# Performance work log

Measured on AMD Instinct MI355X. Metric: run time of the kernel, lower is better.

## Reference

```python
import jax, jax.numpy as jnp
import numpy as np
import math

B, S, D, H = 4, 1024, 2048, 16
DH = D // H          # dim_head = 128
DHID = 128           # dim_hid
DKER = 64            # dim_ker
EPS = 1e-6


def setup_inputs() -> dict:
    key = jax.random.key(0)
    ks = jax.random.split(key, 12)
    a1 = math.sqrt(6.0 / (DH + DHID))
    a2 = math.sqrt(6.0 / (DKER + DHID))
    a3 = math.sqrt(6.0 / (2 * DKER))
    return {
        "q": jax.random.normal(ks[0], (B, S, D), jnp.float32),
        "k": jax.random.normal(ks[1], (B, S, D), jnp.float32),
        "v": jax.random.normal(ks[2], (B, S, D), jnp.float32),
        "lr_attn_mask": jax.random.randint(ks[3], (B, 1, S, S), 0, 2).astype(bool),
        "sparse_norms_lse": jax.random.normal(ks[4], (B, H, S, 1), jnp.float32),
        "sparse_attn_weights": jax.random.normal(ks[5], (B, H, S, S), jnp.float32),
        "kernel_q_mat1": jax.random.uniform(ks[6], (H, DH, DHID), jnp.float32, -a1, a1),
        "kernel_k_mat1": jax.random.uniform(ks[7], (H, DH, DHID), jnp.float32, -a1, a1),
        "kernel_q_mat2": jax.random.uniform(ks[8], (H, DHID, DKER), jnp.float32, -a2, a2),
        "kernel_k_mat2": jax.random.uniform(ks[9], (H, DHID, DKER), jnp.float32, -a2, a2),
        "interaction_k": jax.random.uniform(ks[10], (H, DKER, DKER), jnp.float32, -a3, a3),
        "scalingD": jnp.ones((1, H, 1, DKER), jnp.float32) * 1e-4,
        "scalingD2": jnp.ones((1, H, 1, DKER), jnp.float32) * 1e-4,
        "lambda_constant": 1,
    }


def _gelu(x):
    # torch F.gelu default = exact (erf) gelu
    return jax.nn.gelu(x, approximate=False)


def reference(q, k, v, lr_attn_mask, sparse_norms_lse, sparse_attn_weights,
              kernel_q_mat1, kernel_k_mat1, kernel_q_mat2, kernel_k_mat2,
              interaction_k, scalingD, scalingD2, lambda_constant):
    # split heads: [B,S,D] -> [B,H,S,DH]
    qh = q.reshape(B, S, H, DH).transpose(0, 2, 1, 3)
    kh = k.reshape(B, S, H, DH).transpose(0, 2, 1, 3)
    vh = v.reshape(B, S, H, DH).transpose(0, 2, 1, 3)

    # learned kernel feature maps (dropout=0 -> identity)
    qf = _gelu(jnp.einsum('bhsd,hde->bhse', qh, kernel_q_mat1))
    qf = _gelu(jnp.einsum('bhse,hef->bhsf', qf, kernel_q_mat2))

    kf = _gelu(jnp.einsum('bhsd,hde->bhse', kh, kernel_k_mat1))
    kf = jnp.abs(scalingD) * _gelu(jnp.einsum('bhse,hef->bhsf', kf, kernel_k_mat2))
    kf = kf + jnp.einsum('bhse,hef->bhsf', kf, interaction_k) * scalingD2

    # low-rank (kernelized) scores, masked. [B,H,S,S]
    scores = jnp.einsum('bhse,bhte->bhst', jnp.abs(qf), jnp.abs(kf))
    m = lr_attn_mask.astype(scores.dtype)  # [B,1,S,S] broadcasts
    scores = m * scores

    # log-domain merge with external sparse attention
    lr_norms_lse = jnp.log(scores.sum(axis=-1, keepdims=True) + EPS)
    norm_factor_lse = jnp.logaddexp(lr_norms_lse, sparse_norms_lse)
    logits = jnp.log(scores + EPS) * m + (1.0 - m) * sparse_attn_weights
    attn = jnp.exp(logits - norm_factor_lse)

    out = jnp.einsum('bhst,bhtd->bhsd', attn, vh)
    return out.transpose(0, 2, 1, 3).reshape(B, S, D)
```

## Files before the change

kernel.cpp:

```cpp
#include <hip/hip_runtime.h>


typedef __bf16 bf16_t;
typedef __attribute__((ext_vector_type(8))) __bf16 bf16x8;
typedef __attribute__((ext_vector_type(4))) float f32x4;

#define MFMA(a, b, c) __builtin_amdgcn_mfma_f32_16x16x32_bf16((a), (b), (c), 0, 0, 0)

typedef __attribute__((address_space(3))) void as3_void;
typedef __attribute__((address_space(1))) const void as1_void;
static __device__ __forceinline__ void gload16(const void* g, void* l) {
    __builtin_amdgcn_global_load_lds((as1_void*)g, (as3_void*)l, 16, 0, 0);
}

static __device__ __forceinline__ float gelu_exact(float x) {
    return 0.5f * x * (1.0f + erff(x * 0.70710678118654752f));
}

static __device__ __forceinline__ unsigned pack_bf16(float a, float b) {
    bf16_t x = (bf16_t)a, y = (bf16_t)b;
    unsigned short ux = __builtin_bit_cast(unsigned short, x);
    unsigned short uy = __builtin_bit_cast(unsigned short, y);
    return (unsigned)ux | ((unsigned)uy << 16);
}

__global__ __launch_bounds__(256) void conv_weights_kernel(
    const float* __restrict__ wq1, const float* __restrict__ wk1,
    const float* __restrict__ wq2, const float* __restrict__ wk2,
    const float* __restrict__ iK,
    bf16_t* __restrict__ wq1t, bf16_t* __restrict__ wk1t,
    bf16_t* __restrict__ wq2t, bf16_t* __restrict__ wk2t,
    bf16_t* __restrict__ iKt)
{
    const int idx = blockIdx.x * 256 + threadIdx.x;
    if (idx < 16 * 128 * 128) {
        int h = idx >> 14, e = (idx >> 7) & 127, d = idx & 127;
        wq1t[idx] = (bf16_t)wq1[(h << 14) + (d << 7) + e];
        wk1t[idx] = (bf16_t)wk1[(h << 14) + (d << 7) + e];
    }
    if (idx < 16 * 64 * 128) {
        int h = idx >> 13, f = (idx >> 7) & 63, e = idx & 127;
        wq2t[idx] = (bf16_t)wq2[(h << 13) + (e << 6) + f];
        wk2t[idx] = (bf16_t)wk2[(h << 13) + (e << 6) + f];
    }
    if (idx < 16 * 64 * 64) {
        int h = idx >> 12, g = (idx >> 6) & 63, f = idx & 63;
        iKt[idx] = (bf16_t)iK[(h << 12) + (f << 6) + g];
    }
}

__global__ __launch_bounds__(256) void prep_kernel(
    const float* __restrict__ q, const float* __restrict__ k,
    const float* __restrict__ v, const unsigned char* __restrict__ mask8,
    const bf16_t* __restrict__ wq1t, const bf16_t* __restrict__ wq2t,
    const bf16_t* __restrict__ wk1t, const bf16_t* __restrict__ wk2t,
    const bf16_t* __restrict__ iKt,
    const float* __restrict__ sD, const float* __restrict__ sD2,
    bf16_t* __restrict__ qf, bf16_t* __restrict__ kf,
    bf16_t* __restrict__ vT, unsigned char* __restrict__ mprep)
{
    __shared__ char smem[44032];
    const int bxg = blockIdx.x;
    const int tid = threadIdx.x;

    if (bxg < 1024) {
        __shared__ int mflag;
        if (tid == 0) {
            unsigned a = 0;
            for (int i = 0; i < 64; ++i) a |= mask8[4 * i + 1];
            mflag = (a == 0) ? 1 : 0;
        }
        __syncthreads();
        const size_t base = ((size_t)bxg * 256 + tid) * 16;
        if (mflag) {
            const int* mi = (const int*)mask8;
            uint4 r;
            unsigned bs[4];
#pragma unroll
            for (int j = 0; j < 4; ++j) {
                int4 vv = *reinterpret_cast<const int4*>(&mi[base + j * 4]);
                bs[j] = (vv.x ? 1u : 0u) | ((vv.y ? 1u : 0u) << 8) |
                        ((vv.z ? 1u : 0u) << 16) | ((vv.w ? 1u : 0u) << 24);
            }
            r.x = bs[0]; r.y = bs[1]; r.z = bs[2]; r.w = bs[3];
            *reinterpret_cast<uint4*>(&mprep[base]) = r;
        } else {
            uint4 vv = *reinterpret_cast<const uint4*>(&mask8[base]);
            uint4 r;
            unsigned* pv = (unsigned*)&vv;
            unsigned* pr = (unsigned*)&r;
#pragma unroll
            for (int j = 0; j < 4; ++j) {
                unsigned x = pv[j], o = 0;
#pragma unroll
                for (int kk = 0; kk < 4; ++kk)
                    o |= (((x >> (8 * kk)) & 255u) ? 1u : 0u) << (8 * kk);
                pr[j] = o;
            }
            *reinterpret_cast<uint4*>(&mprep[base]) = r;
        }
        return;
    }

    if (bxg < 2048) {
        typedef bf16_t tr_t[72];
        tr_t* tr = reinterpret_cast<tr_t*>(smem);
        const int idv = bxg - 1024;
        const int bh = idv & 63, b = bh >> 4, h = bh & 15;
        const int tt = idv >> 6;
        const int t0 = tt * 64;
#pragma unroll
        for (int i = 0; i < 8; ++i) {
            int f4 = tid + 256 * i;
            int t = f4 >> 5, c4 = f4 & 31;
            const float4 vv = *reinterpret_cast<const float4*>(
                &v[((size_t)b * 1024 + t0 + t) * 2048 + h * 128 + c4 * 4]);
            tr[c4 * 4 + 0][t] = (bf16_t)vv.x;
            tr[c4 * 4 + 1][t] = (bf16_t)vv.y;
            tr[c4 * 4 + 2][t] = (bf16_t)vv.z;
            tr[c4 * 4 + 3][t] = (bf16_t)vv.w;
        }
        __syncthreads();
#pragma unroll
        for (int i = 0; i < 32; ++i) {
            int e = tid + 256 * i;
            int d = e >> 6, tl = e & 63;
            vT[(((size_t)bh * 16 + tt) * 128 + d) * 64 + tl] = tr[d][tl];
        }
        return;
    }

    {
        typedef bf16_t row136[136];
        typedef bf16_t row72[72];
        row136* xa = reinterpret_cast<row136*>(smem);
        row136* h1 = reinterpret_cast<row136*>(smem + 17408);
        row72*  k2 = reinterpret_cast<row72*>(smem + 34816);

        const int idf = bxg - 2048;
        const int lane = tid & 63, w = tid >> 6;
        const int lr = lane & 15, lg = lane >> 4;
        const int row0 = (idf & 63) * 64;
        const int h = (idf >> 6) & 15;
        const int path = idf >> 10;

        const float* X = path ? k : q;
        const bf16_t* w1t = path ? wk1t : wq1t;
        const bf16_t* w2t = path ? wk2t : wq2t;
        bf16_t* outp = path ? kf : qf;

#pragma unroll
        for (int i = 0; i < 8; ++i) {
            int f4 = tid + 256 * i;
            int r = f4 >> 5, c4 = f4 & 31;
            const float4 vv = *reinterpret_cast<const float4*>(
                &X[(size_t)(row0 + r) * 2048 + h * 128 + c4 * 4]);
            xa[r][c4 * 4 + 0] = (bf16_t)vv.x;
            xa[r][c4 * 4 + 1] = (bf16_t)vv.y;
            xa[r][c4 * 4 + 2] = (bf16_t)vv.z;
            xa[r][c4 * 4 + 3] = (bf16_t)vv.w;
        }
        __syncthreads();

        bf16x8 a1[4];
#pragma unroll
        for (int kk = 0; kk < 4; ++kk)
            a1[kk] = *reinterpret_cast<const bf16x8*>(&xa[w * 16 + lr][kk * 32 + lg * 8]);
#pragma unroll
        for (int nt = 0; nt < 8; ++nt) {
            f32x4 acc = {0.f, 0.f, 0.f, 0.f};
#pragma unroll
            for (int kk = 0; kk < 4; ++kk) {
                bf16x8 bfr = *reinterpret_cast<const bf16x8*>(
                    &w1t[(size_t)h * 16384 + (nt * 16 + lr) * 128 + kk * 32 + lg * 8]);
                acc = MFMA(a1[kk], bfr, acc);
            }
#pragma unroll
            for (int r = 0; r < 4; ++r)
                h1[w * 16 + lg * 4 + r][nt * 16 + lr] = (bf16_t)gelu_exact(acc[r]);
        }
        __syncthreads();

        bf16x8 a2[4];
#pragma unroll
        for (int kk = 0; kk < 4; ++kk)
            a2[kk] = *reinterpret_cast<const bf16x8*>(&h1[w * 16 + lr][kk * 32 + lg * 8]);

        if (path == 0) {
#pragma unroll
            for (int nt = 0; nt < 4; ++nt) {
                f32x4 acc = {0.f, 0.f, 0.f, 0.f};
#pragma unroll
                for (int kk = 0; kk < 4; ++kk) {
                    bf16x8 bfr = *reinterpret_cast<const bf16x8*>(
                        &w2t[(size_t)h * 8192 + (nt * 16 + lr) * 128 + kk * 32 + lg * 8]);
                    acc = MFMA(a2[kk], bfr, acc);
                }
#pragma unroll
                for (int r = 0; r < 4; ++r) {
                    int n = row0 + w * 16 + lg * 4 + r;
                    int bb = n >> 10, s = n & 1023;
                    outp[(((size_t)bb * 16 + h) * 1024 + s) * 64 + nt * 16 + lr] =
                        (bf16_t)fabsf(gelu_exact(acc[r]));
                }
            }
        } else {
#pragma unroll
            for (int nt = 0; nt < 4; ++nt) {
                f32x4 acc = {0.f, 0.f, 0.f, 0.f};
#pragma unroll
                for (int kk = 0; kk < 4; ++kk) {
                    bf16x8 bfr = *reinterpret_cast<const bf16x8*>(
                        &w2t[(size_t)h * 8192 + (nt * 16 + lr) * 128 + kk * 32 + lg * 8]);
                    acc = MFMA(a2[kk], bfr, acc);
                }
#pragma unroll
                for (int r = 0; r < 4; ++r) {
                    int f = nt * 16 + lr;
                    k2[w * 16 + lg * 4 + r][f] =
                        (bf16_t)(fabsf(sD[h * 64 + f]) * gelu_exact(acc[r]));
                }
            }
            __syncthreads();
            bf16x8 a3[2];
#pragma unroll
            for (int kk = 0; kk < 2; ++kk)
                a3[kk] = *reinterpret_cast<const bf16x8*>(&k2[w * 16 + lr][kk * 32 + lg * 8]);
#pragma unroll
            for (int nt = 0; nt < 4; ++nt) {
                f32x4 acc = {0.f, 0.f, 0.f, 0.f};
#pragma unroll
                for (int kk = 0; kk < 2; ++kk) {
                    bf16x8 bfr = *reinterpret_cast<const bf16x8*>(
                        &iKt[(size_t)h * 4096 + (nt * 16 + lr) * 64 + kk * 32 + lg * 8]);
                    acc = MFMA(a3[kk], bfr, acc);
                }
#pragma unroll
                for (int r = 0; r < 4; ++r) {
                    int row = w * 16 + lg * 4 + r;
                    int g = nt * 16 + lr;
                    float base = (float)k2[row][g];
                    float kv = fabsf(base + acc[r] * sD2[h * 64 + g]);
                    int n = row0 + row;
                    int bb = n >> 10, s = n & 1023;
                    outp[(((size_t)bb * 16 + h) * 1024 + s) * 64 + g] = (bf16_t)kv;
                }
            }
        }
    }
}

__global__ __launch_bounds__(256, 3) void attn_cv_kernel(
    const bf16_t* __restrict__ qf, const bf16_t* __restrict__ kf,
    const bf16_t* __restrict__ vT,
    const unsigned char* __restrict__ mprep,
    const float* __restrict__ saw, const float* __restrict__ lse,
    float* __restrict__ out)
{
    __shared__ bf16_t vbuf[3][128 * 64];

    const int tid = threadIdx.x;
    const int lane = tid & 63, w = tid >> 6;
    const int lr = lane & 15, lg = lane >> 4;

    const int di = blockIdx.y * 16 + blockIdx.x;
    const int xcd = di & 7, rr = di >> 3;
    const int bh = xcd + 8 * (rr >> 4);
    const int s0 = (rr & 15) * 64;
    const int b = bh >> 4, h = bh & 15;

    const int srow = s0 + w * 16 + lr;
    const size_t saw_row = ((size_t)bh << 20) + (size_t)srow * 1024;
    const size_t m_row   = ((size_t)b << 20) + (size_t)srow * 1024;

    const int vrow = tid >> 3;
    const int vcol8 = (tid & 7) ^ (vrow & 7);
    const bf16_t* vt_bh = vT + (size_t)bh * 131072;
    const bf16_t* kf_bh = kf + (size_t)bh * 65536;

    bf16x8 aq0, aq1;
    {
        const size_t qb = ((size_t)bh * 1024 + srow) * 64;
        aq0 = *reinterpret_cast<const bf16x8*>(&qf[qb + lg * 8]);
        aq1 = *reinterpret_cast<const bf16x8*>(&qf[qb + 32 + lg * 8]);
    }

    const f32x4 fzero = {0.f, 0.f, 0.f, 0.f};
    f32x4 oacc[8];
#pragma unroll
    for (int i = 0; i < 8; ++i) oacc[i] = fzero;
    float rs = 0.f;


#define STAGE_VT(BUF, TILE)                                                      \
    {                                                                            \
        const bf16_t* vg = vt_bh + (size_t)(TILE) * 8192 + vcol8 * 8;            \
        char* lb = (char*)&vbuf[BUF][0] + w * 1024;                              \
        _Pragma("unroll")                                                        \
        for (int j = 0; j < 4; ++j)                                              \
            gload16(vg + (size_t)(32 * j + vrow) * 64, lb + j * 4096);           \
    }

#define LOAD_KF(TILE, KR)                                                        \
    {                                                                            \
        _Pragma("unroll")                                                        \
        for (int nt = 0; nt < 4; ++nt) {                                         \
            const size_t kb = ((size_t)(TILE) * 64 + nt * 16 + lr) * 64;         \
            KR[nt * 2]     = *reinterpret_cast<const bf16x8*>(&kf_bh[kb + lg * 8]); \
            KR[nt * 2 + 1] = *reinterpret_cast<const bf16x8*>(&kf_bh[kb + 32 + lg * 8]); \
        }                                                                        \
    }

#define LOAD_SAW(TILE, SS, MM)                                                   \
    {                                                                            \
        _Pragma("unroll")                                                        \
        for (int nt = 0; nt < 4; ++nt) {                                         \
            SS[nt] = *reinterpret_cast<const f32x4*>(                            \
                &saw[saw_row + (size_t)(TILE) * 64 + nt * 16 + lg * 4]);         \
            MM[nt] = *reinterpret_cast<const unsigned*>(                         \
                &mprep[m_row + (size_t)(TILE) * 64 + nt * 16 + lg * 4]);         \
        }                                                                        \
    }

#define QKT_MERGE(KR, SS, MM)                                                    \
    {                                                                            \
        _Pragma("unroll")                                                        \
        for (int nt = 0; nt < 4; ++nt) {                                         \
            f32x4 acc = fzero;                                                   \
            acc = MFMA(KR[nt * 2], aq0, acc);                                    \
            acc = MFMA(KR[nt * 2 + 1], aq1, acc);                                \
            const unsigned mm = MM[nt];                                          \
            float v0, v1, v2, v3;                                                \
            v0 = (mm & 255u)         ? (acc[0] + 1e-6f) : __expf(SS[nt][0]);     \
            rs += (mm & 255u)         ? acc[0] : 0.f;                            \
            v1 = ((mm >> 8) & 255u)  ? (acc[1] + 1e-6f) : __expf(SS[nt][1]);     \
            rs += ((mm >> 8) & 255u)  ? acc[1] : 0.f;                            \
            v2 = ((mm >> 16) & 255u) ? (acc[2] + 1e-6f) : __expf(SS[nt][2]);     \
            rs += ((mm >> 16) & 255u) ? acc[2] : 0.f;                            \
            v3 = (mm >> 24)          ? (acc[3] + 1e-6f) : __expf(SS[nt][3]);     \
            rs += (mm >> 24)          ? acc[3] : 0.f;                            \
            pk[nt * 2]     = pack_bf16(v0, v1);                                  \
            pk[nt * 2 + 1] = pack_bf16(v2, v3);                                  \
        }                                                                        \
    }

#define REDIST()                                                                 \
    {                                                                            \
        const int srcA = lr + ((lg & 1) << 5);                                   \
        const int srcB = srcA + 16;                                              \
        const bool sel = (lg < 2);                                               \
        const unsigned a0 = __shfl(pk[0], srcA, 64);                             \
        const unsigned a1 = __shfl(pk[1], srcA, 64);                             \
        const unsigned a2 = __shfl(pk[2], srcA, 64);                             \
        const unsigned a3 = __shfl(pk[3], srcA, 64);                             \
        const unsigned b0 = __shfl(pk[0], srcB, 64);                             \
        const unsigned b1 = __shfl(pk[1], srcB, 64);                             \
        const unsigned b2 = __shfl(pk[2], srcB, 64);                             \
        const unsigned b3 = __shfl(pk[3], srcB, 64);                             \
        f0w.x = sel ? a0 : a2;  f0w.y = sel ? a1 : a3;                           \
        f0w.z = sel ? b0 : b2;  f0w.w = sel ? b1 : b3;                           \
        const unsigned c4 = __shfl(pk[4], srcA, 64);                             \
        const unsigned c5 = __shfl(pk[5], srcA, 64);                             \
        const unsigned c6 = __shfl(pk[6], srcA, 64);                             \
        const unsigned c7 = __shfl(pk[7], srcA, 64);                             \
        const unsigned d4 = __shfl(pk[4], srcB, 64);                             \
        const unsigned d5 = __shfl(pk[5], srcB, 64);                             \
        const unsigned d6 = __shfl(pk[6], srcB, 64);                             \
        const unsigned d7 = __shfl(pk[7], srcB, 64);                             \
        f1w.x = sel ? c4 : c6;  f1w.y = sel ? c5 : c7;                           \
        f1w.z = sel ? d4 : d6;  f1w.w = sel ? d5 : d7;                           \
    }

#define PV(CUR)                                                                  \
    {                                                                            \
        bf16x8 pf0 = __builtin_bit_cast(bf16x8, f0w);                            \
        bf16x8 pf1 = __builtin_bit_cast(bf16x8, f1w);                            \
        __builtin_amdgcn_s_setprio(1);                                           \
        _Pragma("unroll")                                                        \
        for (int dt = 0; dt < 8; ++dt) {                                         \
            const int row = dt * 16 + lr;                                        \
            const char* vb = (const char*)&vbuf[CUR][0] + row * 128;             \
            const int sw = (row & 7) * 16;                                       \
            bf16x8 v0 = *reinterpret_cast<const bf16x8*>(vb + ((lg * 16) ^ sw)); \
            bf16x8 v1 = *reinterpret_cast<const bf16x8*>(vb + ((64 + lg * 16) ^ sw)); \
            oacc[dt] = MFMA(v0, pf0, oacc[dt]);                                  \
            oacc[dt] = MFMA(v1, pf1, oacc[dt]);                                  \
        }                                                                        \
        __builtin_amdgcn_s_setprio(0);                                           \
    }

#define FULL_PHASE(CIDX, SIDX, I, KRC, SSC, MMC, KRN, SSN, MMN)                  \
    {                                                                            \
        LOAD_KF((I) + 1, KRN);                                                   \
        LOAD_SAW((I) + 1, SSN, MMN);                                             \
        STAGE_VT(SIDX, (I) + 2);                                                 \
        __builtin_amdgcn_sched_barrier(0);                                       \
        asm volatile("s_waitcnt vmcnt(24)" ::: "memory");                        \
        __builtin_amdgcn_s_barrier();                                            \
        __builtin_amdgcn_sched_barrier(0);                                       \
        QKT_MERGE(KRC, SSC, MMC);                                                \
        REDIST();                                                                \
        __builtin_amdgcn_sched_barrier(0);                                       \
        PV(CIDX);                                                                \
        __builtin_amdgcn_sched_barrier(0);                                       \
        __builtin_amdgcn_s_barrier();                                            \
    }

    f32x4 sawA[4], sawB[4];
    unsigned muA[4], muB[4];
    bf16x8 kfA[8], kfB[8];
    unsigned pk[8];
    uint4 f0w, f1w;

    LOAD_KF(0, kfA);
    LOAD_SAW(0, sawA, muA);
    STAGE_VT(0, 0);
    STAGE_VT(1, 1);

    int c0 = 0, c1 = 1, c2 = 2;
    for (int i = 0; i < 14; i += 2) {
        FULL_PHASE(c0, c2, i,     kfA, sawA, muA, kfB, sawB, muB);
        FULL_PHASE(c1, c0, i + 1, kfB, sawB, muB, kfA, sawA, muA);
        const int t_ = c0; c0 = c2; c2 = c1; c1 = t_;
    }

    {
        LOAD_KF(15, kfB);
        LOAD_SAW(15, sawB, muB);
        __builtin_amdgcn_sched_barrier(0);
        asm volatile("s_waitcnt vmcnt(20)" ::: "memory");
        __builtin_amdgcn_s_barrier();
        __builtin_amdgcn_sched_barrier(0);
        QKT_MERGE(kfA, sawA, muA);
        REDIST();
        __builtin_amdgcn_sched_barrier(0);
        PV(c0);
        __builtin_amdgcn_sched_barrier(0);
        __builtin_amdgcn_s_barrier();
    }
    {
        asm volatile("s_waitcnt vmcnt(0)" ::: "memory");
        __builtin_amdgcn_s_barrier();
        __builtin_amdgcn_sched_barrier(0);
        QKT_MERGE(kfB, sawB, muB);
        REDIST();
        __builtin_amdgcn_sched_barrier(0);
        PV(c1);
    }

    rs += __shfl_xor(rs, 16);
    rs += __shfl_xor(rs, 32);
    const float invden =
        1.0f / (rs + 1e-6f + __expf(lse[(size_t)bh * 1024 + srow]));

    const size_t ob = ((size_t)b * 1024 + srow) * 2048 + h * 128 + lg * 4;
#pragma unroll
    for (int dt = 0; dt < 8; ++dt) {
        f32x4 o;
        o[0] = oacc[dt][0] * invden;
        o[1] = oacc[dt][1] * invden;
        o[2] = oacc[dt][2] * invden;
        o[3] = oacc[dt][3] * invden;
        *reinterpret_cast<f32x4*>(&out[ob + dt * 16]) = o;
    }
#undef STAGE_VT
#undef LOAD_KF
#undef LOAD_SAW
#undef QKT_MERGE
#undef REDIST
#undef PV
#undef FULL_PHASE
}

extern "C" void kernel_launch(void* const* d_in, const int* in_sizes, int n_in,
                              void* d_out, int out_size, void* d_ws, size_t ws_size,
                              hipStream_t stream)
{
    const float* q   = (const float*)d_in[0];
    const float* k   = (const float*)d_in[1];
    const float* v   = (const float*)d_in[2];
    const unsigned char* mask = (const unsigned char*)d_in[3];
    const float* lse = (const float*)d_in[4];
    const float* saw = (const float*)d_in[5];
    const float* wq1 = (const float*)d_in[6];
    const float* wk1 = (const float*)d_in[7];
    const float* wq2 = (const float*)d_in[8];
    const float* wk2 = (const float*)d_in[9];
    const float* iK  = (const float*)d_in[10];
    const float* sD  = (const float*)d_in[11];
    const float* sD2 = (const float*)d_in[12];
    float* out = (float*)d_out;

    bf16_t* wsb  = (bf16_t*)d_ws;
    bf16_t* wq1t = wsb;
    bf16_t* wk1t = wq1t + 262144;
    bf16_t* wq2t = wk1t + 262144;
    bf16_t* wk2t = wq2t + 131072;
    bf16_t* iKt  = wk2t + 131072;
    bf16_t* qf   = iKt  + 65536;
    bf16_t* kf   = qf   + 4194304;
    bf16_t* vT   = kf   + 4194304;
    unsigned char* mprep = (unsigned char*)(vT + 8388608);

    conv_weights_kernel<<<dim3(1024), dim3(256), 0, stream>>>(
        wq1, wk1, wq2, wk2, iK, wq1t, wk1t, wq2t, wk2t, iKt);
    prep_kernel<<<dim3(4096), dim3(256), 0, stream>>>(
        q, k, v, mask, wq1t, wq2t, wk1t, wk2t, iKt, sD, sD2, qf, kf, vT, mprep);
    attn_cv_kernel<<<dim3(16, 64), dim3(256), 0, stream>>>(
        qf, kf, vT, mprep, saw, lse, out);
}
```

Before: 232.6 us.

## Precompute exp of sparse weights merged with mask into bf16 tile layout

The prep kernel now reads the fp32 sparse attention weights and the mask once. It writes a single bf16 tensor in a tiled layout: exp(weight) where the mask is off, and a -1 sentinel where the mask is on. The attention kernel then loads this compact bf16 tensor instead of the fp32 weights plus a separate mask byte array, and drops its per-element exp. This halves the bytes the attention loop has to stream, but the extra write and read-back of the intermediate raises total global memory traffic. Storing exp values in bf16 also adds rounding error.

```diff
diff --git a/kernel.cpp b/kernel.cpp
--- a/kernel.cpp
+++ b/kernel.cpp
@@ -22,6 +22,10 @@
     unsigned short ux = __builtin_bit_cast(unsigned short, x);
     unsigned short uy = __builtin_bit_cast(unsigned short, y);
     return (unsigned)ux | ((unsigned)uy << 16);
+}
+
+static __device__ __forceinline__ float bf16u_to_f32(unsigned short u) {
+    return __uint_as_float((unsigned)u << 16);
 }
 
 __global__ __launch_bounds__(256) void conv_weights_kernel(
@@ -52,12 +56,13 @@
 __global__ __launch_bounds__(256) void prep_kernel(
     const float* __restrict__ q, const float* __restrict__ k,
     const float* __restrict__ v, const unsigned char* __restrict__ mask8,
+    const float* __restrict__ saw,
     const bf16_t* __restrict__ wq1t, const bf16_t* __restrict__ wq2t,
     const bf16_t* __restrict__ wk1t, const bf16_t* __restrict__ wk2t,
     const bf16_t* __restrict__ iKt,
     const float* __restrict__ sD, const float* __restrict__ sD2,
     bf16_t* __restrict__ qf, bf16_t* __restrict__ kf,
-    bf16_t* __restrict__ vT, unsigned char* __restrict__ mprep)
+    bf16_t* __restrict__ vT, bf16_t* __restrict__ pt)
 {
     __shared__ char smem[44032];
     const int bxg = blockIdx.x;
@@ -71,33 +76,41 @@
             mflag = (a == 0) ? 1 : 0;
         }
         __syncthreads();
-        const size_t base = ((size_t)bxg * 256 + tid) * 16;
-        if (mflag) {
-            const int* mi = (const int*)mask8;
-            uint4 r;
-            unsigned bs[4];
-#pragma unroll
-            for (int j = 0; j < 4; ++j) {
-                int4 vv = *reinterpret_cast<const int4*>(&mi[base + j * 4]);
-                bs[j] = (vv.x ? 1u : 0u) | ((vv.y ? 1u : 0u) << 8) |
-                        ((vv.z ? 1u : 0u) << 16) | ((vv.w ? 1u : 0u) << 24);
+        const bool mask_is_int = (mflag != 0);
+        const int* mask32 = (const int*)mask8;
+
+        const int bh = bxg & 63, b = bh >> 4;
+        const int s0 = (bxg >> 6) * 64;
+        const int w_ = tid >> 6, l = tid & 63;
+        const size_t sawb = ((size_t)bh << 20) + (size_t)s0 * 1024;
+        const size_t mb = ((size_t)b << 20) + (size_t)s0 * 1024;
+
+        for (int tc = 0; tc < 4; ++tc) {
+#pragma unroll
+            for (int i = 0; i < 16; ++i) {
+                const int r = i * 4 + w_;
+                const int col = tc * 256 + l * 4;
+                const size_t e = (size_t)r * 1024 + col;
+                const float4 sv = *reinterpret_cast<const float4*>(&saw[sawb + e]);
+                int m0, m1, m2, m3;
+                if (mask_is_int) {
+                    const int4 mv = *reinterpret_cast<const int4*>(&mask32[mb + e]);
+                    m0 = mv.x; m1 = mv.y; m2 = mv.z; m3 = mv.w;
+                } else {
+                    const uchar4 mv = *reinterpret_cast<const uchar4*>(&mask8[mb + e]);
+                    m0 = mv.x; m1 = mv.y; m2 = mv.z; m3 = mv.w;
+                }
+                bf16_t o[4];
+                o[0] = m0 ? (bf16_t)(-1.0f) : (bf16_t)__expf(sv.x);
+                o[1] = m1 ? (bf16_t)(-1.0f) : (bf16_t)__expf(sv.y);
+                o[2] = m2 ? (bf16_t)(-1.0f) : (bf16_t)__expf(sv.z);
+                o[3] = m3 ? (bf16_t)(-1.0f) : (bf16_t)__expf(sv.w);
+                const int ttg = tc * 4 + (l >> 4);
+                const int tin = (l & 15) * 4;
+                *reinterpret_cast<uint2*>(
+                    &pt[(((size_t)bh * 16 + ttg) * 1024 + s0 + r) * 64 + tin]) =
+                    *reinterpret_cast<const uint2*>(o);
             }
-            r.x = bs[0]; r.y = bs[1]; r.z = bs[2]; r.w = bs[3];
-            *reinterpret_cast<uint4*>(&mprep[base]) = r;
-        } else {
-            uint4 vv = *reinterpret_cast<const uint4*>(&mask8[base]);
-            uint4 r;
-            unsigned* pv = (unsigned*)&vv;
-            unsigned* pr = (unsigned*)&r;
-#pragma unroll
-            for (int j = 0; j < 4; ++j) {
-                unsigned x = pv[j], o = 0;
-#pragma unroll
-                for (int kk = 0; kk < 4; ++kk)
-                    o |= (((x >> (8 * kk)) & 255u) ? 1u : 0u) << (8 * kk);
-                pr[j] = o;
-            }
-            *reinterpret_cast<uint4*>(&mprep[base]) = r;
         }
         return;
     }
@@ -252,10 +265,8 @@
 
 __global__ __launch_bounds__(256, 3) void attn_cv_kernel(
     const bf16_t* __restrict__ qf, const bf16_t* __restrict__ kf,
-    const bf16_t* __restrict__ vT,
-    const unsigned char* __restrict__ mprep,
-    const float* __restrict__ saw, const float* __restrict__ lse,
-    float* __restrict__ out)
+    const bf16_t* __restrict__ vT, const bf16_t* __restrict__ pt,
+    const float* __restrict__ lse, float* __restrict__ out)
 {
     __shared__ bf16_t vbuf[3][128 * 64];
 
@@ -270,13 +281,13 @@
     const int b = bh >> 4, h = bh & 15;
 
     const int srow = s0 + w * 16 + lr;
-    const size_t saw_row = ((size_t)bh << 20) + (size_t)srow * 1024;
-    const size_t m_row   = ((size_t)b << 20) + (size_t)srow * 1024;
 
     const int vrow = tid >> 3;
     const int vcol8 = (tid & 7) ^ (vrow & 7);
     const bf16_t* vt_bh = vT + (size_t)bh * 131072;
     const bf16_t* kf_bh = kf + (size_t)bh * 65536;
+    const unsigned short* ptp = (const unsigned short*)pt
+        + ((size_t)bh * 16) * 65536 + (size_t)srow * 64;
 
     bf16x8 aq0, aq1;
     {
@@ -311,34 +322,34 @@
         }                                                                        \
     }
 
-#define LOAD_SAW(TILE, SS, MM)                                                   \
+#define LOAD_PT(TILE, PP)                                                        \
     {                                                                            \
         _Pragma("unroll")                                                        \
-        for (int nt = 0; nt < 4; ++nt) {                                         \
-            SS[nt] = *reinterpret_cast<const f32x4*>(                            \
-                &saw[saw_row + (size_t)(TILE) * 64 + nt * 16 + lg * 4]);         \
-            MM[nt] = *reinterpret_cast<const unsigned*>(                         \
-                &mprep[m_row + (size_t)(TILE) * 64 + nt * 16 + lg * 4]);         \
-        }                                                                        \
-    }
-
-#define QKT_MERGE(KR, SS, MM)                                                    \
+        for (int nt = 0; nt < 4; ++nt)                                           \
+            PP[nt] = *reinterpret_cast<const ushort4*>(                          \
+                &ptp[(size_t)(TILE) * 65536 + nt * 16 + lg * 4]);                \
+    }
+
+#define QKT_MERGE(KR, PP)                                                        \
     {                                                                            \
         _Pragma("unroll")                                                        \
         for (int nt = 0; nt < 4; ++nt) {                                         \
             f32x4 acc = fzero;                                                   \
             acc = MFMA(KR[nt * 2], aq0, acc);                                    \
             acc = MFMA(KR[nt * 2 + 1], aq1, acc);                                \
-            const unsigned mm = MM[nt];                                          \
+            const float pe0 = bf16u_to_f32(PP[nt].x);                            \
+            const float pe1 = bf16u_to_f32(PP[nt].y);                            \
+            const float pe2 = bf16u_to_f32(PP[nt].z);                            \
+            const float pe3 = bf16u_to_f32(PP[nt].w);                            \
             float v0, v1, v2, v3;                                                \
-            v0 = (mm & 255u)         ? (acc[0] + 1e-6f) : __expf(SS[nt][0]);     \
-            rs += (mm & 255u)         ? acc[0] : 0.f;                            \
-            v1 = ((mm >> 8) & 255u)  ? (acc[1] + 1e-6f) : __expf(SS[nt][1]);     \
-            rs += ((mm >> 8) & 255u)  ? acc[1] : 0.f;                            \
-            v2 = ((mm >> 16) & 255u) ? (acc[2] + 1e-6f) : __expf(SS[nt][2]);     \
-            rs += ((mm >> 16) & 255u) ? acc[2] : 0.f;                            \
-            v3 = (mm >> 24)          ? (acc[3] + 1e-6f) : __expf(SS[nt][3]);     \
-            rs += (mm >> 24)          ? acc[3] : 0.f;                            \
+            v0 = (pe0 < 0.f) ? (acc[0] + 1e-6f) : pe0;                           \
+            rs += (pe0 < 0.f) ? acc[0] : 0.f;                                    \
+            v1 = (pe1 < 0.f) ? (acc[1] + 1e-6f) : pe1;                           \
+            rs += (pe1 < 0.f) ? acc[1] : 0.f;                                    \
+            v2 = (pe2 < 0.f) ? (acc[2] + 1e-6f) : pe2;                           \
+            rs += (pe2 < 0.f) ? acc[2] : 0.f;                                    \
+            v3 = (pe3 < 0.f) ? (acc[3] + 1e-6f) : pe3;                           \
+            rs += (pe3 < 0.f) ? acc[3] : 0.f;                                    \
             pk[nt * 2]     = pack_bf16(v0, v1);                                  \
             pk[nt * 2 + 1] = pack_bf16(v2, v3);                                  \
         }                                                                        \
@@ -389,16 +400,16 @@
         __builtin_amdgcn_s_setprio(0);                                           \
     }
 
-#define FULL_PHASE(CIDX, SIDX, I, KRC, SSC, MMC, KRN, SSN, MMN)                  \
+#define FULL_PHASE(CIDX, SIDX, I, KRC, PPC, KRN, PPN)                            \
     {                                                                            \
         LOAD_KF((I) + 1, KRN);                                                   \
-        LOAD_SAW((I) + 1, SSN, MMN);                                             \
+        LOAD_PT((I) + 1, PPN);                                                   \
         STAGE_VT(SIDX, (I) + 2);                                                 \
         __builtin_amdgcn_sched_barrier(0);                                       \
-        asm volatile("s_waitcnt vmcnt(24)" ::: "memory");                        \
+        asm volatile("s_waitcnt vmcnt(20)" ::: "memory");                        \
         __builtin_amdgcn_s_barrier();                                            \
         __builtin_amdgcn_sched_barrier(0);                                       \
-        QKT_MERGE(KRC, SSC, MMC);                                                \
+        QKT_MERGE(KRC, PPC);                                                     \
         REDIST();                                                                \
         __builtin_amdgcn_sched_barrier(0);                                       \
         PV(CIDX);                                                                \
@@ -406,32 +417,31 @@
         __builtin_amdgcn_s_barrier();                                            \
     }
 
-    f32x4 sawA[4], sawB[4];
-    unsigned muA[4], muB[4];
+    ushort4 ptA[4], ptB[4];
     bf16x8 kfA[8], kfB[8];
     unsigned pk[8];
     uint4 f0w, f1w;
 
     LOAD_KF(0, kfA);
-    LOAD_SAW(0, sawA, muA);
+    LOAD_PT(0, ptA);
     STAGE_VT(0, 0);
     STAGE_VT(1, 1);
 
     int c0 = 0, c1 = 1, c2 = 2;
     for (int i = 0; i < 14; i += 2) {
-        FULL_PHASE(c0, c2, i,     kfA, sawA, muA, kfB, sawB, muB);
-        FULL_PHASE(c1, c0, i + 1, kfB, sawB, muB, kfA, sawA, muA);
+        FULL_PHASE(c0, c2, i,     kfA, ptA, kfB, ptB);
+        FULL_PHASE(c1, c0, i + 1, kfB, ptB, kfA, ptA);
         const int t_ = c0; c0 = c2; c2 = c1; c1 = t_;
     }
 
     {
         LOAD_KF(15, kfB);
-        LOAD_SAW(15, sawB, muB);
+        LOAD_PT(15, ptB);
         __builtin_amdgcn_sched_barrier(0);
-        asm volatile("s_waitcnt vmcnt(20)" ::: "memory");
+        asm volatile("s_waitcnt vmcnt(16)" ::: "memory");
         __builtin_amdgcn_s_barrier();
         __builtin_amdgcn_sched_barrier(0);
-        QKT_MERGE(kfA, sawA, muA);
+        QKT_MERGE(kfA, ptA);
         REDIST();
         __builtin_amdgcn_sched_barrier(0);
         PV(c0);
@@ -442,7 +452,7 @@
         asm volatile("s_waitcnt vmcnt(0)" ::: "memory");
         __builtin_amdgcn_s_barrier();
         __builtin_amdgcn_sched_barrier(0);
-        QKT_MERGE(kfB, sawB, muB);
+        QKT_MERGE(kfB, ptB);
         REDIST();
         __builtin_amdgcn_sched_barrier(0);
         PV(c1);
@@ -465,7 +475,7 @@
     }
 #undef STAGE_VT
 #undef LOAD_KF
-#undef LOAD_SAW
+#undef LOAD_PT
 #undef QKT_MERGE
 #undef REDIST
 #undef PV
@@ -500,12 +510,12 @@
     bf16_t* qf   = iKt  + 65536;
     bf16_t* kf   = qf   + 4194304;
     bf16_t* vT   = kf   + 4194304;
-    unsigned char* mprep = (unsigned char*)(vT + 8388608);
+    bf16_t* pt   = vT   + 8388608;
 
     conv_weights_kernel<<<dim3(1024), dim3(256), 0, stream>>>(
         wq1, wk1, wq2, wk2, iK, wq1t, wk1t, wq2t, wk2t, iKt);
     prep_kernel<<<dim3(4096), dim3(256), 0, stream>>>(
-        q, k, v, mask, wq1t, wq2t, wk1t, wk2t, iKt, sD, sD2, qf, kf, vT, mprep);
+        q, k, v, mask, saw, wq1t, wq2t, wk1t, wk2t, iKt, sD, sD2, qf, kf, vT, pt);
     attn_cv_kernel<<<dim3(16, 64), dim3(256), 0, stream>>>(
-        qf, kf, vT, mprep, saw, lse, out);
-}
+        qf, kf, vT, pt, lse, out);
+}
```

Result: slower. 284.2 us (+22.2%).
